# Kernel tuning notes

Hardware: AMD Instinct MI355X
Metric: run time of the kernel (lower is better)

The kernel has to match this reference:

```python
import jax, jax.numpy as jnp
import numpy as np

DIMVEC = 196
POS_LABEL = 98
NBLABELS = 10
M = 128
UNIHIGH = 0.012
BATCH = 8192


def setup_inputs() -> dict:
    key = jax.random.key(0)
    ks = jax.random.split(key, 6)
    # input features: one 2-vector per site, normalized to unit norm (cos/sin style)
    x = jax.random.uniform(ks[0], (BATCH, DIMVEC, 2), dtype=jnp.float32)
    x = x / jnp.linalg.norm(x, axis=-1, keepdims=True)
    # MPS tensors, uniform(0, unihigh) as in the original construct_tensornetwork
    w0 = jax.random.uniform(ks[1], (2, M), dtype=jnp.float32) * UNIHIGH
    w_left = jax.random.uniform(ks[2], (POS_LABEL - 1, 2, M, M), dtype=jnp.float32) * UNIHIGH
    w_label = jax.random.uniform(ks[3], (2, M, M, NBLABELS), dtype=jnp.float32) * UNIHIGH
    w_right = jax.random.uniform(ks[4], (DIMVEC - 2 - POS_LABEL, 2, M, M), dtype=jnp.float32) * UNIHIGH
    w_end = jax.random.uniform(ks[5], (2, M), dtype=jnp.float32) * UNIHIGH
    return {"x": x, "w0": w0, "w_left": w_left, "w_label": w_label,
            "w_right": w_right, "w_end": w_end}


def reference(x, w0, w_left, w_label, w_right, w_end):
    b, d, _ = x.shape
    m = w0.shape[1]

    # left boundary: contract physical leg of site 0 -> [B, m]
    left = x[:, 0, :] @ w0

    # sweep sites 1 .. pos_label-1: left'[b,n] = sum_{p,mm} x[b,p] left[b,mm] W[p,mm,n]
    def lstep(carry, inp):
        W, xi = inp                       # W: [2,m,m], xi: [B,2]
        o = (xi[:, :, None] * carry[:, None, :]).reshape(b, 2 * m)  # [B, 2m]
        return o @ W.reshape(2 * m, m), None                        # GEMM B x 2m x m

    left, _ = jax.lax.scan(lstep, left,
                           (w_left, jnp.swapaxes(x[:, 1:POS_LABEL], 0, 1)))

    # right boundary: contract physical leg of last site -> [B, m]
    right = x[:, -1, :] @ w_end

    # sweep sites dimvec-2 .. pos_label+1 (reverse):
    # right'[b,mm] = sum_{p,n} x[b,p] right[b,n] W[p,mm,n]
    def rstep(carry, inp):
        W, xi = inp
        o = (xi[:, :, None] * carry[:, None, :]).reshape(b, 2 * m)  # [B, 2m]
        Wt = jnp.swapaxes(W, 1, 2).reshape(2 * m, m)                # [p,n,mm] -> [2m, m]
        return o @ Wt, None

    right, _ = jax.lax.scan(rstep, right,
                            (w_right, jnp.swapaxes(x[:, POS_LABEL + 1:d - 1], 0, 1)),
                            reverse=True)

    # label site: contract left bond first (small intermediate [B,2,m,L])
    xl = x[:, POS_LABEL, :]                                   # [B, 2]
    z = jnp.einsum('bm,pmnl->bpnl', left, w_label)             # [B,2,m,L]
    leftL = jnp.einsum('bpnl,bp->bnl', z, xl)                  # [B,m,L]

    # close the chain with the right environment -> [B, nblabels]
    return jnp.einsum('bnl,bn->bl', leftL, right)
```

## Files before the change

kernel.cpp:

```cpp
#include <hip/hip_runtime.h>

#define BATCH 8192
#define MDIM 128
#define NL 10
#define LSTEPS 97
#define RSTEPS 96
#define NSTEPS 193
#define DIM 196
#define POSL 98

typedef _Float16 half8 __attribute__((ext_vector_type(8)));
typedef float float16v __attribute__((ext_vector_type(16)));

#define BARRIER_LGKM() asm volatile("s_waitcnt lgkmcnt(0)\ns_barrier" ::: "memory")

#define MFMA16 __builtin_amdgcn_mfma_f32_32x32x16_f16

__global__ __launch_bounds__(256) void transpose_x(const float* __restrict__ x,
                                                   float2* __restrict__ xT) {
    __shared__ float tx[64][65];
    __shared__ float ty[64][65];
    int p0 = blockIdx.x * 32;
    int b0 = blockIdx.y * 64;
    int tid = threadIdx.x;

    int r = tid >> 2, q = tid & 3;
    const float* src = x + ((size_t)(b0 + r) * DIM + p0 + q * 8) * 2;
#pragma unroll
    for (int j = 0; j < 8; ++j) {
        int pp = q * 8 + j;
        if (p0 + pp < DIM) {
            float2 v = *(const float2*)(src + j * 2);
            tx[r][pp] = v.x;
            ty[r][pp] = v.y;
        }
    }
    __syncthreads();

    int pr = tid >> 3, cb = (tid & 7) * 8;
    if (p0 + pr < DIM) {
        float2* dst = xT + (size_t)(p0 + pr) * BATCH + b0 + cb;
#pragma unroll
        for (int j = 0; j < 8; ++j) {
            float2 v;
            v.x = tx[cb + j][pr];
            v.y = ty[cb + j][pr];
            dst[j] = v;
        }
    }
}

__global__ __launch_bounds__(256) void pack_w(const float* __restrict__ w_left,
                                              const float* __restrict__ w_right,
                                              _Float16* __restrict__ pw) {
    int g = blockIdx.x >> 2;
    int nt = blockIdx.x & 3;
    int tid = threadIdx.x;
    int l = tid & 63;
    int kq = tid >> 6;
    int hi = l >> 5;
    int n = nt * 32 + (l & 31);
#pragma unroll
    for (int p = 0; p < 4; ++p) {
        int kt = p * 4 + kq;
        int k0 = kt * 16 + hi * 8;
        half8 hv;
        if (g < LSTEPS) {
            const float* base = w_left + (size_t)g * 2 * MDIM * MDIM;
#pragma unroll
            for (int j = 0; j < 8; ++j)
                hv[j] = (_Float16)base[(size_t)(k0 + j) * MDIM + n];
        } else {
            int t = g - LSTEPS;
            int s = k0 >> 7;
            int a0 = k0 & 127;
            const float* row = w_right + (size_t)(RSTEPS - 1 - t) * 2 * MDIM * MDIM
                             + (size_t)s * MDIM * MDIM + (size_t)n * MDIM + a0;
#pragma unroll
            for (int j = 0; j < 8; ++j) hv[j] = (_Float16)row[j];
        }
        *(half8*)(pw + (size_t)(g * 64 + nt * 16 + kt) * 512 + l * 8) = hv;
    }
}

__global__ __launch_bounds__(256) void pack_label(const float* __restrict__ w_label,
                                                  _Float16* __restrict__ gp) {
    int ct = blockIdx.x;
    int tid = threadIdx.x;
    int l = tid & 63;
    int kq = tid >> 6;
    int hi = l >> 5;
    int outcol = ct * 32 + (l & 31);
    int n = outcol & 127;
    int lab = outcol >> 7;
#pragma unroll
    for (int p2 = 0; p2 < 4; ++p2) {
        int kt = p2 * 4 + kq;
        int k0 = kt * 16 + hi * 8;
        int p = k0 >> 7;
        int m0 = k0 & 127;
        half8 hv;
#pragma unroll
        for (int j = 0; j < 8; ++j)
            hv[j] = (_Float16)w_label[(((size_t)p * MDIM + m0 + j) * MDIM + n) * NL + lab];
        *(half8*)(gp + (size_t)(ct * 16 + kt) * 512 + l * 8) = hv;
    }
}


#define CHAIN_MFMA_BLOCK(AF, SRC)                                            \
    half8 bf0[8], bf1[8];                                                    \
    _Pragma("unroll")                                                        \
    for (int q = 0; q < 8; ++q) {                                            \
        int nb = q * 2 + hi;                                                 \
        int phys = nb ^ (bl & 15);                                           \
        bf0[q] = *(const half8*)&cbuf[SRC][bl * 128 + phys * 8];             \
        bf1[q] = *(const half8*)&cbuf[SRC][(bl + 32) * 128 + phys * 8];      \
    }                                                                        \
    float16v a00 = {}, a01 = {}, a10 = {}, a11 = {};                         \
    _Pragma("unroll")                                                        \
    for (int kt = 0; kt < 6; ++kt) {                                         \
        a00 = MFMA16(AF[kt], bf0[kt], a00, 0, 0, 0);                         \
        a10 = MFMA16(AF[kt], bf1[kt], a10, 0, 0, 0);                         \
        a01 = MFMA16(AF[kt + 8], bf0[kt], a01, 0, 0, 0);                     \
        a11 = MFMA16(AF[kt + 8], bf1[kt], a11, 0, 0, 0);                     \
    }                                                                        \
    a00 = MFMA16(AF[6], bf0[6], a00, 0, 0, 0);                               \
    a01 = MFMA16(AF[14], bf0[6], a01, 0, 0, 0);                              \
    a00 = MFMA16(AF[7], bf0[7], a00, 0, 0, 0);                               \
    a01 = MFMA16(AF[15], bf0[7], a01, 0, 0, 0);                              \
    a10 = MFMA16(AF[6], bf1[6], a10, 0, 0, 0);                               \
    a11 = MFMA16(AF[14], bf1[6], a11, 0, 0, 0);                              \
    a10 = MFMA16(AF[7], bf1[7], a10, 0, 0, 0);                               \
    a11 = MFMA16(AF[15], bf1[7], a11, 0, 0, 0);

#define EPI_RG(DST, XC, A_LO, A_HI, ROWOFF)                                  \
    _Pragma("unroll")                                                        \
    for (int rq = 0; rq < 4; ++rq) {                                         \
        int nb = nt * 4 + rq;                                                \
        int phys = nb ^ (bl & 15);                                           \
        union { _Float16 h[4]; uint2 u; } t;                                 \
        _Pragma("unroll")                                                    \
        for (int r = 0; r < 4; ++r)                                          \
            t.h[r] = (_Float16)((XC).x * A_LO[rq * 4 + r]                    \
                              + (XC).y * A_HI[rq * 4 + r]);                  \
        *(uint2*)&cbuf[DST][(bl + ROWOFF) * 128 + phys * 8 + hi * 4] = t.u;  \
    }

#define FINAL_STORE()                                                        \
    _Pragma("unroll")                                                        \
    for (int r = 0; r < 16; ++r) {                                           \
        int n = nt * 32 + (r & 3) + 8 * (r >> 2) + 4 * hi;                   \
        outT[(size_t)n * BATCH + bbase + bl] = xc0.x * a00[r] + xc0.y * a01[r]; \
        outT[(size_t)n * BATCH + bbase + 32 + bl] = xc1.x * a10[r] + xc1.y * a11[r]; \
    }

__global__ __launch_bounds__(256, 1) void chain_mfma(
        const float2* __restrict__ xT, const float* __restrict__ w0,
        const float* __restrict__ w_end, const _Float16* __restrict__ pw,
        float* __restrict__ leftT, float* __restrict__ rightT) {
    __shared__ _Float16 cbuf[2][64 * 128];

    int bid = blockIdx.x;
    bool is_left = bid < 128;
    int bbase = (is_left ? bid : bid - 128) * 64;
    int tid = threadIdx.x;
    int l = tid & 63;
    int nt = tid >> 6;
    int bl = l & 31;
    int hi = l >> 5;

    int nsteps = is_left ? LSTEPS : RSTEPS;
    int gbase = is_left ? 0 : LSTEPS;
    float* outT = is_left ? leftT : rightT;

    {
        const float* wst = is_left ? w0 : w_end;
        int pos0 = is_left ? 0 : (DIM - 1);
        int b = tid >> 2;
        const float2 xv0 = xT[(size_t)pos0 * BATCH + bbase + b];
#pragma unroll
        for (int h = 0; h < 4; ++h) {
            int nb = (tid & 3) * 4 + h;
            half8 hv;
#pragma unroll
            for (int j = 0; j < 8; ++j) {
                int n = nb * 8 + j;
                hv[j] = (_Float16)(xv0.x * wst[n] + xv0.y * wst[MDIM + n]);
            }
            int phys = nb ^ (b & 15);
            *(half8*)&cbuf[0][b * 128 + phys * 8] = hv;
        }
    }

    const char* pwb = (const char*)pw + (size_t)(gbase * 64 + nt * 16) * 1024
                    + (size_t)l * 16;
    const float2* xTb = xT + bbase;

    half8 A0[16], A1[16];
#pragma unroll
    for (int kt = 0; kt < 16; ++kt)
        A0[kt] = *(const half8*)(pwb + kt * 1024);
    int p00 = is_left ? 1 : (DIM - 2);
    float2 xc0 = xTb[(size_t)p00 * BATCH + bl];
    float2 xc1 = xTb[(size_t)p00 * BATCH + 32 + bl];

    __syncthreads();

    int npairs = nsteps >> 1;
    bool odd = nsteps & 1;
    int last = nsteps - 1;

#pragma unroll 1
    for (int sp = 0; sp < npairs; ++sp) {
        int s0 = 2 * sp;
        {
            int pnext = is_left ? (2 + s0) : (DIM - 3 - s0);
            float2 xn0 = xTb[(size_t)pnext * BATCH + bl];
            float2 xn1 = xTb[(size_t)pnext * BATCH + 32 + bl];
            const char* pn = pwb + (size_t)(s0 + 1) * 65536;
#pragma unroll
            for (int kt = 0; kt < 16; ++kt)
                A1[kt] = *(const half8*)(pn + kt * 1024);

            CHAIN_MFMA_BLOCK(A0, 0)
            EPI_RG(1, xc0, a00, a01, 0)
            EPI_RG(1, xc1, a10, a11, 32)
            BARRIER_LGKM();
            xc0 = xn0; xc1 = xn1;
        }
        {
            int s1 = s0 + 1;
            int pf = (s0 + 2 <= last) ? (s0 + 2) : last;
            int ppf = is_left ? (1 + pf) : (DIM - 2 - pf);
            float2 xn0 = xTb[(size_t)ppf * BATCH + bl];
            float2 xn1 = xTb[(size_t)ppf * BATCH + 32 + bl];
            const char* pn = pwb + (size_t)pf * 65536;
#pragma unroll
            for (int kt = 0; kt < 16; ++kt)
                A0[kt] = *(const half8*)(pn + kt * 1024);

            CHAIN_MFMA_BLOCK(A1, 1)
            if (s1 == last) {
                FINAL_STORE()
            } else {
                EPI_RG(0, xc0, a00, a01, 0)
                EPI_RG(0, xc1, a10, a11, 32)
                BARRIER_LGKM();
            }
            xc0 = xn0; xc1 = xn1;
        }
    }

    if (odd) {
        CHAIN_MFMA_BLOCK(A0, 0)
        FINAL_STORE()
    }
}

__global__ __launch_bounds__(256, 2) void label_mfma(
        const float2* __restrict__ xT, const _Float16* __restrict__ gp,
        const float* __restrict__ leftT, const float* __restrict__ rightT,
        float* __restrict__ out) {
    __shared__ _Float16 R[32 * 256];
    __shared__ float pl[4][32][5];
    __shared__ float xl_s[32][2];

    int bx = blockIdx.x;
    int bbase = blockIdx.y * 32;
    int tid = threadIdx.x;
    int l = tid & 63, nt = tid >> 6, bl = l & 31, hi = l >> 5;

    if (tid < 32) {
        const float2 v = xT[(size_t)POSL * BATCH + bbase + tid];
        xl_s[tid][0] = v.x; xl_s[tid][1] = v.y;
    }
    __syncthreads();

#pragma unroll
    for (int q = 0; q < 4; ++q) {
        int id = tid + q * 256;
        int m = id >> 3;
        int b4 = (id & 7) * 4;
        float4 v = *(const float4*)&leftT[(size_t)m * BATCH + bbase + b4];
        float vv[4] = {v.x, v.y, v.z, v.w};
#pragma unroll
        for (int bi = 0; bi < 4; ++bi) {
            int b = b4 + bi;
            int kb0 = m >> 3;
            int ph0 = (kb0 & 16) | ((kb0 ^ b) & 15);
            R[b * 256 + ph0 * 8 + (m & 7)] = (_Float16)(xl_s[b][0] * vv[bi]);
            int kb1 = kb0 + 16;
            int ph1 = (kb1 & 16) | ((kb1 ^ b) & 15);
            R[b * 256 + ph1 * 8 + (m & 7)] = (_Float16)(xl_s[b][1] * vv[bi]);
        }
    }

    float rv[16];
#pragma unroll
    for (int r = 0; r < 16; ++r) {
        int n = nt * 32 + (r & 3) + 8 * (r >> 2) + 4 * hi;
        rv[r] = rightT[(size_t)n * BATCH + bbase + bl];
    }
    __syncthreads();

    half8 rf[16];
#pragma unroll
    for (int kt = 0; kt < 16; ++kt) {
        int kb = kt * 2 + hi;
        int ph = (kb & 16) | ((kb ^ bl) & 15);
        rf[kt] = *(const half8*)&R[bl * 256 + ph * 8];
    }

    int l0 = bx * 5;
    float outv[5];
#pragma unroll
    for (int li = 0; li < 5; ++li) {
        int ct = (l0 + li) * 4 + nt;
        float16v acc = {};
#pragma unroll
        for (int kt = 0; kt < 16; ++kt) {
            half8 a = *(const half8*)(gp + (size_t)(ct * 16 + kt) * 512 + l * 8);
            acc = __builtin_amdgcn_mfma_f32_32x32x16_f16(a, rf[kt], acc, 0, 0, 0);
        }
        float p = 0.f;
#pragma unroll
        for (int r = 0; r < 16; ++r) p += acc[r] * rv[r];
        p += __shfl_xor(p, 32, 64);
        outv[li] = p;
    }
    if (hi == 0) {
#pragma unroll
        for (int li = 0; li < 5; ++li) pl[nt][bl][li] = outv[li];
    }
    __syncthreads();
    if (tid < 160) {
        int b = tid / 5, li = tid % 5;
        out[(size_t)(bbase + b) * NL + l0 + li] =
            pl[0][b][li] + pl[1][b][li] + pl[2][b][li] + pl[3][b][li];
    }
}

extern "C" void kernel_launch(void* const* d_in, const int* in_sizes, int n_in,
                              void* d_out, int out_size, void* d_ws, size_t ws_size,
                              hipStream_t stream) {
    const float* x       = (const float*)d_in[0];
    const float* w0      = (const float*)d_in[1];
    const float* w_left  = (const float*)d_in[2];
    const float* w_label = (const float*)d_in[3];
    const float* w_right = (const float*)d_in[4];
    const float* w_end   = (const float*)d_in[5];

    _Float16* pw = (_Float16*)d_ws;
    _Float16* gp = pw + (size_t)NSTEPS * 64 * 512;
    float* leftT  = (float*)(gp + (size_t)40 * 16 * 512);
    float* rightT = leftT + (size_t)MDIM * BATCH;
    float2* xT    = (float2*)(rightT + (size_t)MDIM * BATCH);

    transpose_x<<<dim3((DIM + 31) / 32, BATCH / 64), 256, 0, stream>>>(x, xT);
    pack_w<<<dim3(NSTEPS * 4), 256, 0, stream>>>(w_left, w_right, pw);
    pack_label<<<dim3(40), 256, 0, stream>>>(w_label, gp);
    chain_mfma<<<dim3(256), 256, 0, stream>>>(xT, w0, w_end, pw, leftT, rightT);
    label_mfma<<<dim3(2, BATCH / 32), 256, 0, stream>>>(xT, gp, leftT, rightT,
                                                        (float*)d_out);
}
```

Baseline: 234.0 us.

## Preload x into LDS and issue weight loads via inline asm with explicit vmcnt waits

Stages all x values the block needs into a shared-memory buffer once at kernel start, so the chain loop no longer issues per-step global loads for x. Weight fragment prefetches are now raw global_load_dwordx4 asm with s_waitcnt vmcnt(16), so the current step waits only for its own fragments while the next step's loads stay in flight. The MFMA ordering is also simplified to a uniform loop. In exchange it adds about 50KB of LDS and a startup load phase. The hand-written asm and vmcnt bookkeeping are fragile if the compiler emits other vector memory ops in between.

```diff
diff --git a/kernel.cpp b/kernel.cpp
--- a/kernel.cpp
+++ b/kernel.cpp
@@ -107,6 +107,42 @@
     }
 }
 
+
+#define LD16(dst, p, ofs) \
+    asm volatile("global_load_dwordx4 %0, %1, off offset:" ofs : "=v"(dst) : "v"(p))
+
+#define ISSUE_A(DST, PN) do {                                  \
+    const char* _p0 = (PN);                                    \
+    LD16(DST[0],  _p0, "0");                                   \
+    LD16(DST[1],  _p0, "1024");                                \
+    LD16(DST[2],  _p0, "2048");                                \
+    LD16(DST[3],  _p0, "3072");                                \
+    const char* _p1 = _p0 + 4096;                              \
+    LD16(DST[4],  _p1, "0");                                   \
+    LD16(DST[5],  _p1, "1024");                                \
+    LD16(DST[6],  _p1, "2048");                                \
+    LD16(DST[7],  _p1, "3072");                                \
+    const char* _p2 = _p0 + 8192;                              \
+    LD16(DST[8],  _p2, "0");                                   \
+    LD16(DST[9],  _p2, "1024");                                \
+    LD16(DST[10], _p2, "2048");                                \
+    LD16(DST[11], _p2, "3072");                                \
+    const char* _p3 = _p0 + 12288;                             \
+    LD16(DST[12], _p3, "0");                                   \
+    LD16(DST[13], _p3, "1024");                                \
+    LD16(DST[14], _p3, "2048");                                \
+    LD16(DST[15], _p3, "3072");                                \
+} while (0)
+
+#define WAIT_A16() do {                                        \
+    asm volatile("s_waitcnt vmcnt(16)" ::: "memory");          \
+    __builtin_amdgcn_sched_barrier(0);                         \
+} while (0)
+
+#define WAIT_A0() do {                                         \
+    asm volatile("s_waitcnt vmcnt(0)" ::: "memory");           \
+    __builtin_amdgcn_sched_barrier(0);                         \
+} while (0)
 
 #define CHAIN_MFMA_BLOCK(AF, SRC)                                            \
     half8 bf0[8], bf1[8];                                                    \
@@ -119,20 +155,12 @@
     }                                                                        \
     float16v a00 = {}, a01 = {}, a10 = {}, a11 = {};                         \
     _Pragma("unroll")                                                        \
-    for (int kt = 0; kt < 6; ++kt) {                                         \
+    for (int kt = 0; kt < 8; ++kt) {                                         \
         a00 = MFMA16(AF[kt], bf0[kt], a00, 0, 0, 0);                         \
         a10 = MFMA16(AF[kt], bf1[kt], a10, 0, 0, 0);                         \
         a01 = MFMA16(AF[kt + 8], bf0[kt], a01, 0, 0, 0);                     \
         a11 = MFMA16(AF[kt + 8], bf1[kt], a11, 0, 0, 0);                     \
-    }                                                                        \
-    a00 = MFMA16(AF[6], bf0[6], a00, 0, 0, 0);                               \
-    a01 = MFMA16(AF[14], bf0[6], a01, 0, 0, 0);                              \
-    a00 = MFMA16(AF[7], bf0[7], a00, 0, 0, 0);                               \
-    a01 = MFMA16(AF[15], bf0[7], a01, 0, 0, 0);                              \
-    a10 = MFMA16(AF[6], bf1[6], a10, 0, 0, 0);                               \
-    a11 = MFMA16(AF[14], bf1[6], a11, 0, 0, 0);                              \
-    a10 = MFMA16(AF[7], bf1[7], a10, 0, 0, 0);                               \
-    a11 = MFMA16(AF[15], bf1[7], a11, 0, 0, 0);
+    }
 
 #define EPI_RG(DST, XC, A_LO, A_HI, ROWOFF)                                  \
     _Pragma("unroll")                                                        \
@@ -160,6 +188,7 @@
         const float* __restrict__ w_end, const _Float16* __restrict__ pw,
         float* __restrict__ leftT, float* __restrict__ rightT) {
     __shared__ _Float16 cbuf[2][64 * 128];
+    __shared__ float2 xbuf[98][64];
 
     int bid = blockIdx.x;
     bool is_left = bid < 128;
@@ -172,13 +201,19 @@
 
     int nsteps = is_left ? LSTEPS : RSTEPS;
     int gbase = is_left ? 0 : LSTEPS;
+    int pbase = is_left ? 0 : 98;
     float* outT = is_left ? leftT : rightT;
+
+    for (int i = tid; i < 98 * 64; i += 256) {
+        int pos = i >> 6, b = i & 63;
+        xbuf[pos][b] = xT[(size_t)(pbase + pos) * BATCH + bbase + b];
+    }
+    __syncthreads();
 
     {
         const float* wst = is_left ? w0 : w_end;
-        int pos0 = is_left ? 0 : (DIM - 1);
         int b = tid >> 2;
-        const float2 xv0 = xT[(size_t)pos0 * BATCH + bbase + b];
+        float2 xv0 = xbuf[is_left ? 0 : 97][b];
 #pragma unroll
         for (int h = 0; h < 4; ++h) {
             int nb = (tid & 3) * 4 + h;
@@ -195,51 +230,38 @@
 
     const char* pwb = (const char*)pw + (size_t)(gbase * 64 + nt * 16) * 1024
                     + (size_t)l * 16;
-    const float2* xTb = xT + bbase;
+
+    __syncthreads();
 
     half8 A0[16], A1[16];
-#pragma unroll
-    for (int kt = 0; kt < 16; ++kt)
-        A0[kt] = *(const half8*)(pwb + kt * 1024);
-    int p00 = is_left ? 1 : (DIM - 2);
-    float2 xc0 = xTb[(size_t)p00 * BATCH + bl];
-    float2 xc1 = xTb[(size_t)p00 * BATCH + 32 + bl];
-
-    __syncthreads();
+    ISSUE_A(A0, pwb);
 
     int npairs = nsteps >> 1;
-    bool odd = nsteps & 1;
+    bool oddtail = nsteps & 1;
     int last = nsteps - 1;
 
 #pragma unroll 1
     for (int sp = 0; sp < npairs; ++sp) {
         int s0 = 2 * sp;
         {
-            int pnext = is_left ? (2 + s0) : (DIM - 3 - s0);
-            float2 xn0 = xTb[(size_t)pnext * BATCH + bl];
-            float2 xn1 = xTb[(size_t)pnext * BATCH + 32 + bl];
-            const char* pn = pwb + (size_t)(s0 + 1) * 65536;
-#pragma unroll
-            for (int kt = 0; kt < 16; ++kt)
-                A1[kt] = *(const half8*)(pn + kt * 1024);
-
+            ISSUE_A(A1, pwb + (size_t)(s0 + 1) * 65536);
+            WAIT_A16();
+            int xi = is_left ? (1 + s0) : (96 - s0);
+            float2 xc0 = xbuf[xi][bl];
+            float2 xc1 = xbuf[xi][32 + bl];
             CHAIN_MFMA_BLOCK(A0, 0)
             EPI_RG(1, xc0, a00, a01, 0)
             EPI_RG(1, xc1, a10, a11, 32)
             BARRIER_LGKM();
-            xc0 = xn0; xc1 = xn1;
         }
         {
             int s1 = s0 + 1;
             int pf = (s0 + 2 <= last) ? (s0 + 2) : last;
-            int ppf = is_left ? (1 + pf) : (DIM - 2 - pf);
-            float2 xn0 = xTb[(size_t)ppf * BATCH + bl];
-            float2 xn1 = xTb[(size_t)ppf * BATCH + 32 + bl];
-            const char* pn = pwb + (size_t)pf * 65536;
-#pragma unroll
-            for (int kt = 0; kt < 16; ++kt)
-                A0[kt] = *(const half8*)(pn + kt * 1024);
-
+            ISSUE_A(A0, pwb + (size_t)pf * 65536);
+            WAIT_A16();
+            int xi = is_left ? (1 + s1) : (96 - s1);
+            float2 xc0 = xbuf[xi][bl];
+            float2 xc1 = xbuf[xi][32 + bl];
             CHAIN_MFMA_BLOCK(A1, 1)
             if (s1 == last) {
                 FINAL_STORE()
@@ -248,11 +270,14 @@
                 EPI_RG(0, xc1, a10, a11, 32)
                 BARRIER_LGKM();
             }
-            xc0 = xn0; xc1 = xn1;
-        }
-    }
-
-    if (odd) {
+        }
+    }
+
+    if (oddtail) {
+        WAIT_A0();
+        int xi = 1 + last;
+        float2 xc0 = xbuf[xi][bl];
+        float2 xc1 = xbuf[xi][32 + bl];
         CHAIN_MFMA_BLOCK(A0, 0)
         FINAL_STORE()
     }
```

Result: slower. 241.8 us (+3.3%).

## Pre-multiply adjacent MPS site pairs into fused 4-block weights to halve chain steps

Applied to the files above, without the earlier changes.

Adds a packing kernel that multiplies consecutive site tensors pairwise (for each physical index pair i,j) with MFMA, producing 128x512 combined weights. The chain kernel then advances two sites per step, scaling the four product blocks by x_a[i]*x_b[j], which halves the number of serial LDS round-trips and barriers. Per step it loads 32 A fragments (double the register pressure) and the total MFMA count stays about the same. It adds a precompute GEMM over weights and an extra rounding of the products to fp16. The leftover odd left site is handled separately.

```diff
diff --git a/kernel.cpp b/kernel.cpp
--- a/kernel.cpp
+++ b/kernel.cpp
@@ -50,36 +50,115 @@
     }
 }
 
-__global__ __launch_bounds__(256) void pack_w(const float* __restrict__ w_left,
-                                              const float* __restrict__ w_right,
-                                              _Float16* __restrict__ pw) {
-    int g = blockIdx.x >> 2;
-    int nt = blockIdx.x & 3;
+__global__ __launch_bounds__(256) void pack_w96(const float* __restrict__ w_left,
+                                                _Float16* __restrict__ pwt) {
+    int nt = blockIdx.x;
     int tid = threadIdx.x;
     int l = tid & 63;
     int kq = tid >> 6;
     int hi = l >> 5;
     int n = nt * 32 + (l & 31);
+    const float* base = w_left + (size_t)96 * 2 * MDIM * MDIM;
 #pragma unroll
     for (int p = 0; p < 4; ++p) {
         int kt = p * 4 + kq;
         int k0 = kt * 16 + hi * 8;
         half8 hv;
-        if (g < LSTEPS) {
-            const float* base = w_left + (size_t)g * 2 * MDIM * MDIM;
-#pragma unroll
-            for (int j = 0; j < 8; ++j)
-                hv[j] = (_Float16)base[(size_t)(k0 + j) * MDIM + n];
+#pragma unroll
+        for (int j = 0; j < 8; ++j)
+            hv[j] = (_Float16)base[(size_t)(k0 + j) * MDIM + n];
+        *(half8*)(pwt + ((size_t)nt * 16 + kt) * 512 + l * 8) = hv;
+    }
+}
+
+__global__ __launch_bounds__(256) void pack_wpair(const float* __restrict__ wl,
+                                                  const float* __restrict__ wr,
+                                                  _Float16* __restrict__ wp) {
+    __shared__ _Float16 P[128][130];
+    int blk = blockIdx.x;
+    int pair = blk >> 2;
+    int ij = blk & 3;
+    int i = ij >> 1, j = ij & 1;
+    bool left = pair < 48;
+    int sp = left ? pair : pair - 48;
+    int tid = threadIdx.x;
+    int l = tid & 63, nt = tid >> 6, bl = l & 31, hi = l >> 5;
+
+    half8 af[8];
+    if (left) {
+        const float* base = wl + (((size_t)(2 * sp + 1) * 2 + j) * 128) * 128;
+#pragma unroll
+        for (int kt = 0; kt < 8; ++kt) {
+            int q0 = kt * 16 + hi * 8;
+#pragma unroll
+            for (int jj = 0; jj < 8; ++jj)
+                af[kt][jj] = (_Float16)base[(size_t)(q0 + jj) * 128 + nt * 32 + bl];
+        }
+    } else {
+        int t1 = 2 * sp + 1;
+        const float* row = wr + ((((size_t)(95 - t1) * 2 + j) * 128)
+                               + nt * 32 + bl) * 128;
+#pragma unroll
+        for (int kt = 0; kt < 8; ++kt) {
+            int q0 = kt * 16 + hi * 8;
+            float4 v0 = *(const float4*)(row + q0);
+            float4 v1 = *(const float4*)(row + q0 + 4);
+            af[kt][0] = (_Float16)v0.x; af[kt][1] = (_Float16)v0.y;
+            af[kt][2] = (_Float16)v0.z; af[kt][3] = (_Float16)v0.w;
+            af[kt][4] = (_Float16)v1.x; af[kt][5] = (_Float16)v1.y;
+            af[kt][6] = (_Float16)v1.z; af[kt][7] = (_Float16)v1.w;
+        }
+    }
+
+#pragma unroll 1
+    for (int mt = 0; mt < 4; ++mt) {
+        half8 bf[8];
+        if (left) {
+            const float* row = wl + ((((size_t)(2 * sp) * 2 + i) * 128)
+                                   + mt * 32 + bl) * 128;
+#pragma unroll
+            for (int kt = 0; kt < 8; ++kt) {
+                int q0 = kt * 16 + hi * 8;
+                float4 v0 = *(const float4*)(row + q0);
+                float4 v1 = *(const float4*)(row + q0 + 4);
+                bf[kt][0] = (_Float16)v0.x; bf[kt][1] = (_Float16)v0.y;
+                bf[kt][2] = (_Float16)v0.z; bf[kt][3] = (_Float16)v0.w;
+                bf[kt][4] = (_Float16)v1.x; bf[kt][5] = (_Float16)v1.y;
+                bf[kt][6] = (_Float16)v1.z; bf[kt][7] = (_Float16)v1.w;
+            }
         } else {
-            int t = g - LSTEPS;
-            int s = k0 >> 7;
-            int a0 = k0 & 127;
-            const float* row = w_right + (size_t)(RSTEPS - 1 - t) * 2 * MDIM * MDIM
-                             + (size_t)s * MDIM * MDIM + (size_t)n * MDIM + a0;
-#pragma unroll
-            for (int j = 0; j < 8; ++j) hv[j] = (_Float16)row[j];
-        }
-        *(half8*)(pw + (size_t)(g * 64 + nt * 16 + kt) * 512 + l * 8) = hv;
+            int t0 = 2 * sp;
+            const float* base = wr + (((size_t)(95 - t0) * 2 + i) * 128) * 128;
+#pragma unroll
+            for (int kt = 0; kt < 8; ++kt) {
+                int q0 = kt * 16 + hi * 8;
+#pragma unroll
+                for (int jj = 0; jj < 8; ++jj)
+                    bf[kt][jj] = (_Float16)base[(size_t)(q0 + jj) * 128
+                                              + mt * 32 + bl];
+            }
+        }
+        float16v d = {};
+#pragma unroll
+        for (int kt = 0; kt < 8; ++kt)
+            d = MFMA16(af[kt], bf[kt], d, 0, 0, 0);
+#pragma unroll
+        for (int r = 0; r < 16; ++r)
+            P[mt * 32 + bl][nt * 32 + (r & 3) + 8 * (r >> 2) + 4 * hi]
+                = (_Float16)d[r];
+    }
+    __syncthreads();
+
+    _Float16* dst = wp + ((size_t)pair * 128 + ij * 32 + nt * 8) * 512
+                  + (size_t)l * 8;
+#pragma unroll
+    for (int kt2 = 0; kt2 < 8; ++kt2) {
+        int m0 = kt2 * 16 + hi * 8;
+        half8 hv;
+#pragma unroll
+        for (int jj = 0; jj < 8; ++jj)
+            hv[jj] = P[m0 + jj][nt * 32 + bl];
+        *(half8*)(dst + (size_t)kt2 * 512) = hv;
     }
 }
 
@@ -107,6 +186,48 @@
     }
 }
 
+
+#define READ_BF_F(SRC, ROWOFF)                                               \
+    half8 bf[8];                                                             \
+    _Pragma("unroll")                                                        \
+    for (int q = 0; q < 8; ++q) {                                            \
+        int nb = q * 2 + hi;                                                 \
+        int phys = nb ^ (bl & 15);                                           \
+        bf[q] = *(const half8*)&cbuf[SRC][(bl + ROWOFF) * 128 + phys * 8];   \
+    }
+
+#define PROD_CHAINS()                                                        \
+    float16v p0 = {}, p1 = {}, p2 = {}, p3 = {};                             \
+    _Pragma("unroll")                                                        \
+    for (int kt = 0; kt < 8; ++kt) {                                         \
+        p0 = MFMA16(A[kt],      bf[kt], p0, 0, 0, 0);                        \
+        p1 = MFMA16(A[kt + 8],  bf[kt], p1, 0, 0, 0);                        \
+        p2 = MFMA16(A[kt + 16], bf[kt], p2, 0, 0, 0);                        \
+        p3 = MFMA16(A[kt + 24], bf[kt], p3, 0, 0, 0);                        \
+    }
+
+#define EPI4(DST, ROWOFF, C00, C01, C10, C11)                                \
+    _Pragma("unroll")                                                        \
+    for (int rq = 0; rq < 4; ++rq) {                                         \
+        int nb = nt * 4 + rq;                                                \
+        int phys = nb ^ (bl & 15);                                           \
+        union { _Float16 h[4]; uint2 u; } t;                                 \
+        _Pragma("unroll")                                                    \
+        for (int r = 0; r < 4; ++r) {                                        \
+            int rr = rq * 4 + r;                                             \
+            t.h[r] = (_Float16)((C00) * p0[rr] + (C01) * p1[rr]              \
+                              + (C10) * p2[rr] + (C11) * p3[rr]);            \
+        }                                                                    \
+        *(uint2*)&cbuf[DST][(bl + ROWOFF) * 128 + phys * 8 + hi * 4] = t.u;  \
+    }
+
+#define FINAL4(ROWOFF, C00, C01, C10, C11)                                   \
+    _Pragma("unroll")                                                        \
+    for (int r = 0; r < 16; ++r) {                                           \
+        int n = nt * 32 + (r & 3) + 8 * (r >> 2) + 4 * hi;                   \
+        outT[(size_t)n * BATCH + bbase + (ROWOFF) + bl] =                    \
+            (C00) * p0[r] + (C01) * p1[r] + (C10) * p2[r] + (C11) * p3[r];   \
+    }
 
 #define CHAIN_MFMA_BLOCK(AF, SRC)                                            \
     half8 bf0[8], bf1[8];                                                    \
@@ -119,32 +240,11 @@
     }                                                                        \
     float16v a00 = {}, a01 = {}, a10 = {}, a11 = {};                         \
     _Pragma("unroll")                                                        \
-    for (int kt = 0; kt < 6; ++kt) {                                         \
+    for (int kt = 0; kt < 8; ++kt) {                                         \
         a00 = MFMA16(AF[kt], bf0[kt], a00, 0, 0, 0);                         \
         a10 = MFMA16(AF[kt], bf1[kt], a10, 0, 0, 0);                         \
         a01 = MFMA16(AF[kt + 8], bf0[kt], a01, 0, 0, 0);                     \
         a11 = MFMA16(AF[kt + 8], bf1[kt], a11, 0, 0, 0);                     \
-    }                                                                        \
-    a00 = MFMA16(AF[6], bf0[6], a00, 0, 0, 0);                               \
-    a01 = MFMA16(AF[14], bf0[6], a01, 0, 0, 0);                              \
-    a00 = MFMA16(AF[7], bf0[7], a00, 0, 0, 0);                               \
-    a01 = MFMA16(AF[15], bf0[7], a01, 0, 0, 0);                              \
-    a10 = MFMA16(AF[6], bf1[6], a10, 0, 0, 0);                               \
-    a11 = MFMA16(AF[14], bf1[6], a11, 0, 0, 0);                              \
-    a10 = MFMA16(AF[7], bf1[7], a10, 0, 0, 0);                               \
-    a11 = MFMA16(AF[15], bf1[7], a11, 0, 0, 0);
-
-#define EPI_RG(DST, XC, A_LO, A_HI, ROWOFF)                                  \
-    _Pragma("unroll")                                                        \
-    for (int rq = 0; rq < 4; ++rq) {                                         \
-        int nb = nt * 4 + rq;                                                \
-        int phys = nb ^ (bl & 15);                                           \
-        union { _Float16 h[4]; uint2 u; } t;                                 \
-        _Pragma("unroll")                                                    \
-        for (int r = 0; r < 4; ++r)                                          \
-            t.h[r] = (_Float16)((XC).x * A_LO[rq * 4 + r]                    \
-                              + (XC).y * A_HI[rq * 4 + r]);                  \
-        *(uint2*)&cbuf[DST][(bl + ROWOFF) * 128 + phys * 8 + hi * 4] = t.u;  \
     }
 
 #define FINAL_STORE()                                                        \
@@ -155,9 +255,10 @@
         outT[(size_t)n * BATCH + bbase + 32 + bl] = xc1.x * a10[r] + xc1.y * a11[r]; \
     }
 
-__global__ __launch_bounds__(256, 1) void chain_mfma(
+__global__ __launch_bounds__(256, 1) void chain_fused(
         const float2* __restrict__ xT, const float* __restrict__ w0,
-        const float* __restrict__ w_end, const _Float16* __restrict__ pw,
+        const float* __restrict__ w_end, const _Float16* __restrict__ wp,
+        const _Float16* __restrict__ pwt,
         float* __restrict__ leftT, float* __restrict__ rightT) {
     __shared__ _Float16 cbuf[2][64 * 128];
 
@@ -170,8 +271,6 @@
     int bl = l & 31;
     int hi = l >> 5;
 
-    int nsteps = is_left ? LSTEPS : RSTEPS;
-    int gbase = is_left ? 0 : LSTEPS;
     float* outT = is_left ? leftT : rightT;
 
     {
@@ -193,66 +292,59 @@
         }
     }
 
-    const char* pwb = (const char*)pw + (size_t)(gbase * 64 + nt * 16) * 1024
-                    + (size_t)l * 16;
+    const char* wpb = (const char*)wp
+                    + ((size_t)(is_left ? 0 : 48) * 131072)
+                    + (size_t)nt * 8192 + (size_t)l * 16;
     const float2* xTb = xT + bbase;
 
-    half8 A0[16], A1[16];
-#pragma unroll
-    for (int kt = 0; kt < 16; ++kt)
-        A0[kt] = *(const half8*)(pwb + kt * 1024);
-    int p00 = is_left ? 1 : (DIM - 2);
-    float2 xc0 = xTb[(size_t)p00 * BATCH + bl];
-    float2 xc1 = xTb[(size_t)p00 * BATCH + 32 + bl];
-
-    __syncthreads();
-
-    int npairs = nsteps >> 1;
-    bool odd = nsteps & 1;
-    int last = nsteps - 1;
+    __syncthreads();
 
 #pragma unroll 1
-    for (int sp = 0; sp < npairs; ++sp) {
-        int s0 = 2 * sp;
+    for (int sp2 = 0; sp2 < 48; ++sp2) {
+        int src = sp2 & 1;
+        int pA = is_left ? (1 + 2 * sp2) : (194 - 2 * sp2);
+        int pB = is_left ? (2 + 2 * sp2) : (193 - 2 * sp2);
+        float2 xa0 = xTb[(size_t)pA * BATCH + bl];
+        float2 xb0 = xTb[(size_t)pB * BATCH + bl];
+        float2 xa1 = xTb[(size_t)pA * BATCH + 32 + bl];
+        float2 xb1 = xTb[(size_t)pB * BATCH + 32 + bl];
+
+        const char* pp = wpb + (size_t)sp2 * 131072;
+        half8 A[32];
+#pragma unroll
+        for (int f = 0; f < 32; ++f)
+            A[f] = *(const half8*)(pp + (size_t)(f >> 3) * 32768
+                                      + (size_t)(f & 7) * 1024);
+
+        bool fin = (!is_left) && (sp2 == 47);
         {
-            int pnext = is_left ? (2 + s0) : (DIM - 3 - s0);
-            float2 xn0 = xTb[(size_t)pnext * BATCH + bl];
-            float2 xn1 = xTb[(size_t)pnext * BATCH + 32 + bl];
-            const char* pn = pwb + (size_t)(s0 + 1) * 65536;
-#pragma unroll
-            for (int kt = 0; kt < 16; ++kt)
-                A1[kt] = *(const half8*)(pn + kt * 1024);
-
-            CHAIN_MFMA_BLOCK(A0, 0)
-            EPI_RG(1, xc0, a00, a01, 0)
-            EPI_RG(1, xc1, a10, a11, 32)
-            BARRIER_LGKM();
-            xc0 = xn0; xc1 = xn1;
+            READ_BF_F(src, 0)
+            PROD_CHAINS()
+            float c00 = xa0.x * xb0.x, c01 = xa0.x * xb0.y;
+            float c10 = xa0.y * xb0.x, c11 = xa0.y * xb0.y;
+            if (fin) { FINAL4(0, c00, c01, c10, c11) }
+            else     { EPI4(src ^ 1, 0, c00, c01, c10, c11) }
         }
         {
-            int s1 = s0 + 1;
-            int pf = (s0 + 2 <= last) ? (s0 + 2) : last;
-            int ppf = is_left ? (1 + pf) : (DIM - 2 - pf);
-            float2 xn0 = xTb[(size_t)ppf * BATCH + bl];
-            float2 xn1 = xTb[(size_t)ppf * BATCH + 32 + bl];
-            const char* pn = pwb + (size_t)pf * 65536;
-#pragma unroll
-            for (int kt = 0; kt < 16; ++kt)
-                A0[kt] = *(const half8*)(pn + kt * 1024);
-
-            CHAIN_MFMA_BLOCK(A1, 1)
-            if (s1 == last) {
-                FINAL_STORE()
-            } else {
-                EPI_RG(0, xc0, a00, a01, 0)
-                EPI_RG(0, xc1, a10, a11, 32)
-                BARRIER_LGKM();
-            }
-            xc0 = xn0; xc1 = xn1;
-        }
-    }
-
-    if (odd) {
+            READ_BF_F(src, 32)
+            PROD_CHAINS()
+            float c00 = xa1.x * xb1.x, c01 = xa1.x * xb1.y;
+            float c10 = xa1.y * xb1.x, c11 = xa1.y * xb1.y;
+            if (fin) { FINAL4(32, c00, c01, c10, c11) }
+            else     { EPI4(src ^ 1, 32, c00, c01, c10, c11) }
+        }
+        if (!fin) BARRIER_LGKM();
+    }
+
+    if (is_left) {
+        const char* pt = (const char*)pwt + (size_t)(nt * 16) * 1024
+                       + (size_t)l * 16;
+        half8 A0[16];
+#pragma unroll
+        for (int kt = 0; kt < 16; ++kt)
+            A0[kt] = *(const half8*)(pt + kt * 1024);
+        float2 xc0 = xTb[(size_t)97 * BATCH + bl];
+        float2 xc1 = xTb[(size_t)97 * BATCH + 32 + bl];
         CHAIN_MFMA_BLOCK(A0, 0)
         FINAL_STORE()
     }
@@ -351,16 +443,19 @@
     const float* w_right = (const float*)d_in[4];
     const float* w_end   = (const float*)d_in[5];
 
-    _Float16* pw = (_Float16*)d_ws;
-    _Float16* gp = pw + (size_t)NSTEPS * 64 * 512;
+    _Float16* wp  = (_Float16*)d_ws;
+    _Float16* pwt = wp + (size_t)96 * 65536;
+    _Float16* gp  = pwt + 32768;
     float* leftT  = (float*)(gp + (size_t)40 * 16 * 512);
     float* rightT = leftT + (size_t)MDIM * BATCH;
     float2* xT    = (float2*)(rightT + (size_t)MDIM * BATCH);
 
     transpose_x<<<dim3((DIM + 31) / 32, BATCH / 64), 256, 0, stream>>>(x, xT);
-    pack_w<<<dim3(NSTEPS * 4), 256, 0, stream>>>(w_left, w_right, pw);
+    pack_w96<<<dim3(4), 256, 0, stream>>>(w_left, pwt);
+    pack_wpair<<<dim3(96 * 4), 256, 0, stream>>>(w_left, w_right, wp);
     pack_label<<<dim3(40), 256, 0, stream>>>(w_label, gp);
-    chain_mfma<<<dim3(256), 256, 0, stream>>>(xT, w0, w_end, pw, leftT, rightT);
+    chain_fused<<<dim3(256), 256, 0, stream>>>(xT, w0, w_end, wp, pwt,
+                                               leftT, rightT);
     label_mfma<<<dim3(2, BATCH / 32), 256, 0, stream>>>(xT, gp, leftT, rightT,
                                                         (float*)d_out);
 }
```

Result: slower. 282.8 us (+20.8%).
